# Kernel optimization log

Hardware: AMD Instinct MI355X
Metric: run time of the kernel (lower is better)

## Reference

```python
import jax, jax.numpy as jnp
import numpy as np

N_QUBITS = 12
DEPTH = 4
OUT_DIM = 2
HID = 64
BATCH = 4096


def _u3(a, b, c):
    """Combined RZ(c) @ RY(b) @ RX(a) single-qubit gate, batched. a,b,c: [B] -> [B,2,2] complex."""
    ca, sa = jnp.cos(a / 2), jnp.sin(a / 2)
    cb, sb = jnp.cos(b / 2), jnp.sin(b / 2)
    RX = jnp.stack([jnp.stack([ca + 0j, -1j * sa], -1),
                    jnp.stack([-1j * sa, ca + 0j], -1)], -2)
    RY = jnp.stack([jnp.stack([cb + 0j, -sb + 0j], -1),
                    jnp.stack([sb + 0j, cb + 0j], -1)], -2)
    ez = jnp.exp(-1j * c / 2)
    zeros = jnp.zeros_like(ez)
    RZ = jnp.stack([jnp.stack([ez, zeros], -1),
                    jnp.stack([zeros, jnp.conj(ez)], -1)], -2)
    return jnp.einsum('bij,bjk,bkl->bil', RZ, RY, RX)


def _apply_1q(psi, U, q):
    """psi: [B]+[2]*n (wire 0 = most significant), U: [B,2,2]."""
    psi = jnp.moveaxis(psi, q + 1, 1)
    shp = psi.shape
    psi = psi.reshape(shp[0], 2, -1)
    psi = jnp.einsum('bij,bjr->bir', U, psi)
    return jnp.moveaxis(psi.reshape(shp), 1, q + 1)


def _apply_cnot(psi, c, t):
    """CNOT with control c, target t on psi [B]+[2]*n."""
    s0 = jax.lax.index_in_dim(psi, 0, axis=c + 1, keepdims=True)
    s1 = jax.lax.index_in_dim(psi, 1, axis=c + 1, keepdims=True)
    s1 = jnp.flip(s1, axis=t + 1)
    return jnp.concatenate([s0, s1], axis=c + 1)


def _circuit_expvals(params):
    """Batched hardware-efficient ansatz state-vector sim.
    params: [B, DEPTH, N_QUBITS, 3] -> PauliZ expvals [B, N_QUBITS]."""
    B = params.shape[0]
    n = N_QUBITS
    psi = jnp.zeros((B, 2 ** n), jnp.complex64).at[:, 0].set(1.0)
    psi = psi.reshape((B,) + (2,) * n)
    for l in range(DEPTH):
        for q in range(n):  # RX, RY, RZ per qubit (fused to one 2x2)
            U = _u3(params[:, l, q, 0], params[:, l, q, 1], params[:, l, q, 2])
            psi = _apply_1q(psi, U, q)
        for q in range(n):   # ring of CNOTs
            psi = _apply_cnot(psi, q, (q + 1) % n)
    probs = (psi.real ** 2 + psi.imag ** 2).reshape(B, 2 ** n)
    idx = jnp.arange(2 ** n)
    bits = (idx[None, :] >> (n - 1 - jnp.arange(n))[:, None]) & 1  # [n, 2^n]
    signs = (1.0 - 2.0 * bits).astype(jnp.float32)
    return probs @ signs.T  # <Z_q> = p(bit=0) - p(bit=1)


def setup_inputs() -> dict:
    key = jax.random.key(0)
    ks = jax.random.split(key, 5)
    n = N_QUBITS
    n_params = DEPTH * n * 3
    def w(k, shape):
        return (jax.random.normal(k, shape, jnp.float32) / np.sqrt(shape[0])).astype(jnp.float32)
    return {
        'noise': jax.random.normal(ks[0], (BATCH, n), jnp.float32),
        'W1': w(ks[1], (n, HID)), 'b1': jnp.zeros((HID,), jnp.float32),
        'W2': w(ks[2], (HID, n_params)), 'b2': jnp.zeros((n_params,), jnp.float32),
        'W3': w(ks[3], (n, HID)), 'b3': jnp.zeros((HID,), jnp.float32),
        'W4': w(ks[4], (HID, OUT_DIM)), 'b4': jnp.zeros((OUT_DIM,), jnp.float32),
    }


def reference(noise, W1, b1, W2, b2, W3, b3, W4, b4):
    h = jnp.tanh(noise @ W1 + b1)
    circ_params = (h @ W2 + b2).reshape(noise.shape[0], DEPTH, N_QUBITS, 3)
    meas = _circuit_expvals(circ_params)          # [B, n_qubits]
    h2 = jnp.tanh(meas @ W3 + b3)
    return h2 @ W4 + b4                            # [B, output_dim]
```

## Files before the change

kernel.cpp:

```cpp
#include <hip/hip_runtime.h>
#include <math.h>

#define NQ  12
#define TPB 256

typedef __attribute__((ext_vector_type(2))) float f2;


struct GF12 { unsigned row[12]; };

constexpr GF12 gf_id(){ GF12 m{}; for(int i=0;i<12;i++) m.row[i]=1u<<i; return m; }
constexpr GF12 gf_mul(const GF12&A,const GF12&B){
  GF12 r{};
  for(int i=0;i<12;i++){ unsigned acc=0;
    for(int k=0;k<12;k++) if((A.row[i]>>k)&1u) acc ^= B.row[k];
    r.row[i]=acc; }
  return r;
}
constexpr unsigned gf_apply(const GF12&A, unsigned x){
  unsigned y=0;
  for(int i=0;i<12;i++) y |= (unsigned)(__builtin_popcount(A.row[i]&x)&1)<<i;
  return y;
}
constexpr GF12 gf_cnot(int q){ GF12 m=gf_id(); int c=11-q, t=11-((q+1)%12); m.row[t]^=(1u<<c); return m; }
constexpr GF12 gf_inv(const GF12&A){
  unsigned a[12], inv[12];
  for(int i=0;i<12;i++){ a[i]=A.row[i]; inv[i]=1u<<i; }
  for(int c=0;c<12;c++){
    int p=-1;
    for(int r2=c;r2<12;r2++) if((a[r2]>>c)&1u){p=r2;break;}
    if(p<0) continue;
    unsigned ta=a[c]; a[c]=a[p]; a[p]=ta;
    unsigned ti=inv[c]; inv[c]=inv[p]; inv[p]=ti;
    for(int r2=0;r2<12;r2++) if(r2!=c && ((a[r2]>>c)&1u)){ a[r2]^=a[c]; inv[r2]^=inv[c]; }
  }
  GF12 R{}; for(int i=0;i<12;i++) R.row[i]=inv[i];
  return R;
}

struct Red { unsigned arr[12]; int hb[12]; int n; };
constexpr unsigned red_reduce(const Red& R, unsigned y){
  for(int i=0;i<R.n;i++) if((y>>R.hb[i])&1u) y ^= R.arr[i];
  return y;
}
constexpr bool red_add(Red& R, unsigned cand){
  unsigned y = red_reduce(R, cand);
  if(!y) return false;
  int h=0;
  for(int b2=11;b2>=1;b2--) if((y>>b2)&1u){ h=b2; break; }
  R.arr[R.n]=y; R.hb[R.n]=h; R.n++;
  return true;
}

struct PairT {
  unsigned M0[4], M1[4];
  unsigned sz[16], gx[16];
  unsigned rB[8], roff[16];
};
struct AllT { PairT pr[6]; unsigned mq[12], uq[12]; bool ok; };

constexpr AllT makeAll(){
  AllT T{}; T.ok=true;
  GF12 D=gf_id(); for(int q=0;q<12;q++) D=gf_mul(gf_cnot(q),D);
  GF12 Cm=gf_id(); for(int q=11;q>=0;q--) Cm=gf_mul(gf_cnot(q),Cm);
  unsigned V[12][4]{},R[12][4]{},rfin[12]{};
  GF12 Mm=gf_id(), Mi=gf_id();
  for(int l=0;l<4;l++){
    for(int q=0;q<12;q++){
      int b=11-q; unsigned v=0;
      for(int j=0;j<12;j++) v|=((Mi.row[j]>>b)&1u)<<j;
      V[l*3+q/4][q&3]=v; R[l*3+q/4][q&3]=Mm.row[b];
    }
    Mm=gf_mul(D,Mm); Mi=gf_mul(Cm,Mi);
  }
  for(int q=0;q<12;q++) rfin[q]=Mm.row[11-q];

  GF12 Sg=gf_id(); Sg.row[1]|=1u<<4; Sg.row[2]|=1u<<5; Sg.row[3]|=1u<<6;

  GF12 Tprev{}, Tprev_inv{};
  for(int m=0;m<6;m++){
    const int p0=2*m, p1=p0+1;
    for(int pp=p0;pp<=p1;pp++) for(int j=0;j<4;j++) for(int i=0;i<4;i++){
      int par=__builtin_popcount(R[pp][j]&V[pp][i])&1;
      if(par!=((i==j)?1:0)) T.ok=false;
    }
    Red S{};
    for(int i=0;i<4;i++){ red_add(S,V[p0][i]); red_add(S,V[p1][i]); }
    for(unsigned x=1;x<4096 && S.n<10;x++) red_add(S,x);
    if(S.n!=10) T.ok=false;
    Red S12=S, RA{}, RB{};
    for(int i=0;i<4;i++){ red_add(RA,V[p0][i]); red_add(RB,V[p1][i]); }
    unsigned B[8]{};
    Red resR{};
    for(int k=0;k<6;k++){
      unsigned pick=0;
      if(m>0){
        unsigned res=(k<4)?(1u<<k):0u;
        for(unsigned hi=(k<4)?0u:1u; hi<256 && !pick; hi++){
          unsigned y=res|(hi<<4);
          unsigned x=gf_apply(Tprev_inv,y);
          if(red_reduce(S,x)) continue;
          if(!red_reduce(RA,x)) continue;
          if(!red_reduce(RB,x)) continue;
          pick=x;
        }
        for(unsigned y=1;y<4096 && !pick;y++){
          unsigned x=gf_apply(Tprev_inv,y);
          if(red_reduce(S,x)) continue;
          if(!red_reduce(RA,x)) continue;
          if(!red_reduce(RB,x)) continue;
          if(k<4){ unsigned rb=y&15u; if(!rb || !red_reduce(resR,rb)) continue; }
          pick=x;
        }
      }
      if(!pick){
        for(unsigned x=1;x<4096 && !pick;x++){
          if(red_reduce(S,x)) continue;
          if(!red_reduce(RA,x)) continue;
          if(!red_reduce(RB,x)) continue;
          pick=x;
        }
      }
      if(!pick){ T.ok=false; pick=1; }
      if(m>0 && k<4){ unsigned rb=gf_apply(Tprev,pick)&15u; if(rb) red_add(resR,rb); }
      red_add(RA,pick); red_add(RB,pick);
      B[k]=pick;
    }
    for(int k=6;k<8;k++){
      unsigned pick=0;
      for(unsigned x=1;x<4096 && !pick;x++) if(red_reduce(S12,x)) pick=x;
      if(!pick){ T.ok=false; pick=1; }
      red_add(S12,pick); B[k]=pick;
    }
    if(S12.n!=12) T.ok=false;
    GF12 Z{};
    for(int i=0;i<12;i++){
      unsigned rr=0;
      for(int k=0;k<4;k++) rr |= ((V[p1][k]>>i)&1u)<<k;
      for(int k=0;k<8;k++) rr |= ((B[k]>>i)&1u)<<(4+k);
      Z.row[i]=rr;
    }
    GF12 Tp=gf_inv(Z);
    { GF12 I2=gf_mul(Tp,Z); for(int i=0;i<12;i++) if(I2.row[i]!=(1u<<i)) T.ok=false; }
    for(int j=0;j<4;j++){
      unsigned m0=0,m1=0;
      for(int k=0;k<8;k++){
        m0 |= (unsigned)(__builtin_popcount(R[p0][j]&B[k])&1)<<k;
        m1 |= (unsigned)(__builtin_popcount(R[p1][j]&B[k])&1)<<k;
      }
      T.pr[m].M0[j]=m0; T.pr[m].M1[j]=m1;
    }
    unsigned zeta[4]{}, gam[4]{};
    for(int i=0;i<4;i++){
      unsigned d=gf_apply(Tp,V[p0][i]);
      if(d>>10) T.ok=false;
      zeta[i]=d&15u; gam[i]=(d>>4)&63u;
    }
    unsigned zmap[16]{}; bool seen[16]{};
    for(int z=0;z<16;z++){
      unsigned zz=0;
      for(int i=0;i<4;i++) if((z>>i)&1) zz^=zeta[i];
      zmap[z]=zz;
      if(seen[zz]) T.ok=false; seen[zz]=true;
    }
    for(int zp=0;zp<16;zp++){
      unsigned src=0;
      for(int z=0;z<16;z++) if(zmap[z]==(unsigned)zp) src=(unsigned)z;
      unsigned gg=0;
      for(int i=0;i<4;i++) if((src>>i)&1) gg^=gam[i];
      T.pr[m].sz[zp]=src; T.pr[m].gx[zp]=gg;
    }
    for(int z=0;z<16;z++){
      unsigned c0=0,c1=0,gg=0,bb=0;
      for(int i=0;i<4;i++){
        if((z>>i)&1){ c0^=V[p0][i]; gg^=gam[i]; }
        if((zmap[z]>>i)&1) c1^=V[p1][i];
      }
      for(int k=0;k<6;k++) if((gg>>k)&1) bb^=B[k];
      if((c0^c1^bb)!=0) T.ok=false;
    }
    if(m>0){
      for(int k=0;k<8;k++) T.pr[m].rB[k]=gf_apply(Tprev,B[k]);
      for(int z=0;z<16;z++){
        unsigned c=0;
        for(int i=0;i<4;i++) if((z>>i)&1) c^=V[p0][i];
        T.pr[m].roff[z]=gf_apply(Tprev,c);
      }
    }
    GF12 Tnew=gf_mul(Sg,Tp), Tnew_inv=gf_mul(Z,Sg);
    { GF12 I2=gf_mul(Tnew,Tnew_inv); for(int i=0;i<12;i++) if(I2.row[i]!=(1u<<i)) T.ok=false; }
    Tprev=Tnew; Tprev_inv=Tnew_inv;
    if(m==5){
      for(int q=0;q<12;q++){
        unsigned u=0,mm=0;
        for(int i=0;i<4;i++) u |= (unsigned)(__builtin_popcount(rfin[q]&V[11][i])&1)<<i;
        for(int k=0;k<8;k++) mm |= (unsigned)(__builtin_popcount(rfin[q]&B[k])&1)<<k;
        T.uq[q]=u; T.mq[q]=mm;
      }
    }
  }
  return T;
}

constexpr AllT hA = makeAll();
static_assert(hA.ok, "GF(2) paired-bpermute table self-check failed");

#define GATE_PK(SS,MM,JJ) do { \
    const int _lb = pl + 4*(JJ); \
    const unsigned _sg = ((unsigned)(__popc((MM) & (unsigned)t) & 1)) << 31; \
    const float _ar = __uint_as_float((unsigned)__builtin_amdgcn_readlane((int)cur, _lb+0)); \
    const float _ai = __uint_as_float(((unsigned)__builtin_amdgcn_readlane((int)cur, _lb+1)) ^ _sg); \
    const float _br = __uint_as_float(((unsigned)__builtin_amdgcn_readlane((int)cur, _lb+2)) ^ _sg); \
    const float _bi = __uint_as_float((unsigned)__builtin_amdgcn_readlane((int)cur, _lb+3)); \
    const f2 A0 = {_ar,_ar}, A1 = {-_ai,_ai}, B0 = {_br,_br}, B1 = {-_bi,_bi}; \
    _Pragma("unroll") \
    for (int s0=0; s0<16; ++s0){ \
      if ((s0 >> (JJ)) & 1) continue; \
      const int s1 = s0 | (1<<(JJ)); \
      const f2 X = SS[s0], Y = SS[s1]; \
      const f2 Xs = __builtin_shufflevector(X,X,1,0); \
      const f2 Ys = __builtin_shufflevector(Y,Y,1,0); \
      SS[s0] = __builtin_elementwise_fma(A0,X, \
               __builtin_elementwise_fma(A1,Xs, \
               __builtin_elementwise_fma(B0,Y, B1*Ys))); \
      SS[s1] = __builtin_elementwise_fma(A0,Y, \
               __builtin_elementwise_fma(-A1,Ys, \
               __builtin_elementwise_fma(-B0,X, B1*Xs))); \
    } \
  } while(0)

template<int M>
__device__ __forceinline__ void do_pair(f2 S[16], f2 Sn[16],
                                        unsigned c0, unsigned c1, unsigned c2,
                                        unsigned t, float2* s2, float4* s4)
{
  constexpr PairT P = hA.pr[M];
  if constexpr (M > 0){
    unsigned base=0;
    #pragma unroll
    for(int k=0;k<8;++k) base ^= ((t>>k)&1u) ? P.rB[k] : 0u;
    #pragma unroll
    for(int z=0;z<16;++z){ float2 v=s2[base ^ P.roff[z]]; S[z].x=v.x; S[z].y=v.y; }
  }
  { constexpr int ci=(2*M)>>2;
    const unsigned cur=(ci==0)?c0:((ci==1)?c1:c2);
    const int pl=((2*M)&3)<<4;
    GATE_PK(S,P.M0[0],0); GATE_PK(S,P.M0[1],1); GATE_PK(S,P.M0[2],2); GATE_PK(S,P.M0[3],3); }
  { const unsigned t4=t<<2;
    #pragma unroll
    for(int zp=0; zp<16; ++zp){
      const int idx=(int)(t4 ^ (P.gx[zp]<<2));
      Sn[zp].x=__uint_as_float((unsigned)__builtin_amdgcn_ds_bpermute(idx,(int)__float_as_uint(S[P.sz[zp]].x)));
      Sn[zp].y=__uint_as_float((unsigned)__builtin_amdgcn_ds_bpermute(idx,(int)__float_as_uint(S[P.sz[zp]].y)));
    } }
  { constexpr int ci=(2*M+1)>>2;
    const unsigned cur=(ci==0)?c0:((ci==1)?c1:c2);
    const int pl=((2*M+1)&3)<<4;
    GATE_PK(Sn,P.M1[0],0); GATE_PK(Sn,P.M1[1],1); GATE_PK(Sn,P.M1[2],2); GATE_PK(Sn,P.M1[3],3); }
  if constexpr (M < 5){
    __syncthreads();
    const unsigned wb=t<<3;
    #pragma unroll
    for(int k=0;k<8;++k)
      s4[wb | ((unsigned)k ^ (t&7u))] =
        make_float4(Sn[2*k].x, Sn[2*k].y, Sn[2*k+1].x, Sn[2*k+1].y);
    __syncthreads();
  }
}

__global__ void __launch_bounds__(TPB, 5)
qgen(const float* __restrict__ noise,
     const float* __restrict__ W1, const float* __restrict__ b1,
     const float* __restrict__ W2, const float* __restrict__ b2,
     const float* __restrict__ W3, const float* __restrict__ b3,
     const float* __restrict__ W4, const float* __restrict__ b4,
     float* __restrict__ out)
{
  __shared__ float2 s2[4096];
  float*  sf=(float*)s2;
  float4* s4=(float4*)s2;

  const unsigned t = threadIdx.x;
  const int b = blockIdx.x;
  const int lane = t & 63;

  if (t < 12) sf[400+t] = noise[b*12+t];
  __syncthreads();
  if (t < 64){
    float a = b1[t];
    #pragma unroll
    for (int k=0;k<12;++k) a = fmaf(sf[400+k], W1[k*64+t], a);
    sf[192+t] = tanhf(a);
  }
  __syncthreads();
  if (t < 144){
    float a = b2[t];
    #pragma unroll 16
    for (int j=0;j<64;++j) a = fmaf(sf[192+j], W2[j*144+t], a);
    sf[256+t] = a;
  }
  __syncthreads();
  if (t < 48){
    float aa = sf[256+3*t+0]*0.5f, bb = sf[256+3*t+1]*0.5f, c = sf[256+3*t+2]*0.5f;
    float sa,ca,sb,cb,sc2,cc;
    __sincosf(aa,&sa,&ca); __sincosf(bb,&sb,&cb); __sincosf(c,&sc2,&cc);
    float A=cb*ca, B=sb*sa, Cc=sb*ca, Dd=cb*sa;
    s4[t] = make_float4(fmaf(cc,A,  sc2*B),  fmaf(cc,B, -sc2*A),
                        fmaf(-cc,Cc,-sc2*Dd), fmaf(sc2,Cc,-cc*Dd));
  }
  __syncthreads();
  const unsigned* su=(const unsigned*)s2;
  const unsigned cu0=su[lane], cu1=su[64+lane], cu2=su[128+lane];
  __syncthreads();

  f2 S[16], Sn[16];
  #pragma unroll
  for(int k=0;k<16;++k){ S[k].x=0.f; S[k].y=0.f; }
  if(t==0) S[0].x=1.0f;

  do_pair<0>(S,Sn,cu0,cu1,cu2,t,s2,s4);
  do_pair<1>(S,Sn,cu0,cu1,cu2,t,s2,s4);
  do_pair<2>(S,Sn,cu0,cu1,cu2,t,s2,s4);
  do_pair<3>(S,Sn,cu0,cu1,cu2,t,s2,s4);
  do_pair<4>(S,Sn,cu0,cu1,cu2,t,s2,s4);
  do_pair<5>(S,Sn,cu0,cu1,cu2,t,s2,s4);

  float H[16];
  #pragma unroll
  for(int z=0;z<16;++z) H[z]=fmaf(Sn[z].x,Sn[z].x, Sn[z].y*Sn[z].y);
  #pragma unroll
  for(int st=1;st<16;st<<=1){
    #pragma unroll
    for(int z=0;z<16;++z){
      if(z & st) continue;
      float a0=H[z], a1=H[z|st];
      H[z]=a0+a1; H[z|st]=a0-a1;
    }
  }
  float acc[12];
  #pragma unroll
  for(int q=0;q<12;++q){
    const unsigned ls=((unsigned)(__popc(hA.mq[q]&t)&1))<<31;
    acc[q]=__uint_as_float(__float_as_uint(H[hA.uq[q]])^ls);
  }

  __syncthreads();
  const int wv=t>>6;
  #pragma unroll
  for(int q=0;q<12;++q){
    float v=acc[q];
    #pragma unroll
    for(int off=32;off>0;off>>=1) v += __shfl_down(v,off,64);
    if(lane==0) sf[wv*12+q]=v;
  }
  __syncthreads();
  if(t<12) sf[64+t]=sf[t]+sf[12+t]+sf[24+t]+sf[36+t];
  __syncthreads();

  if(t<64){
    float a=b3[t];
    #pragma unroll
    for(int k=0;k<12;++k) a=fmaf(sf[64+k],W3[k*64+t],a);
    float h2=tanhf(a);
    float p0=h2*W4[2*t+0], p1=h2*W4[2*t+1];
    #pragma unroll
    for(int off=32;off>0;off>>=1){ p0+=__shfl_down(p0,off,64); p1+=__shfl_down(p1,off,64); }
    if(t==0){ out[2*b+0]=p0+b4[0]; out[2*b+1]=p1+b4[1]; }
  }
}

extern "C" void kernel_launch(void* const* d_in, const int* in_sizes, int n_in,
                              void* d_out, int out_size, void* d_ws, size_t ws_size,
                              hipStream_t stream)
{
  const float* noise=(const float*)d_in[0];
  const float* W1=(const float*)d_in[1];
  const float* b1=(const float*)d_in[2];
  const float* W2=(const float*)d_in[3];
  const float* b2=(const float*)d_in[4];
  const float* W3=(const float*)d_in[5];
  const float* b3=(const float*)d_in[6];
  const float* W4=(const float*)d_in[7];
  const float* b4=(const float*)d_in[8];
  float* out=(float*)d_out;
  const int batch=in_sizes[0]/NQ;
  qgen<<<batch,TPB,0,stream>>>(noise,W1,b1,W2,b2,W3,b3,W4,b4,out);
}
```

Baseline: 200.4 us.

## Switch state-vector sim from radix-16 to radix-8 per thread with 512 threads

Each block now uses 512 threads holding 8 amplitudes each instead of 256 threads holding 16. Qubits are grouped in threes rather than fours, giving 8 paired stages instead of 6, and the GF(2) relabeling tables are regenerated for that grouping. The aim is to cut register pressure and raise per-block parallelism, hiding latency and allowing more waves per CU. The cost is more LDS exchange rounds and block-wide barriers, plus a wider final cross-wave reduction.

```diff
diff --git a/kernel.cpp b/kernel.cpp
--- a/kernel.cpp
+++ b/kernel.cpp
@@ -2,7 +2,7 @@
 #include <math.h>
 
 #define NQ  12
-#define TPB 256
+#define TPB 512
 
 typedef __attribute__((ext_vector_type(2))) float f2;
 
@@ -53,44 +53,55 @@
 }
 
 struct PairT {
-  unsigned M0[4], M1[4];
-  unsigned sz[16], gx[16];
-  unsigned rB[8], roff[16];
+  unsigned M0[3], M1[3];
+  unsigned sz[8], gx[8];
+  unsigned rB[9], roff[8];
 };
-struct AllT { PairT pr[6]; unsigned mq[12], uq[12]; bool ok; };
+struct AllT { PairT pr[8]; unsigned mq[12], uq[12]; bool ok; };
 
 constexpr AllT makeAll(){
   AllT T{}; T.ok=true;
   GF12 D=gf_id(); for(int q=0;q<12;q++) D=gf_mul(gf_cnot(q),D);
   GF12 Cm=gf_id(); for(int q=11;q>=0;q--) Cm=gf_mul(gf_cnot(q),Cm);
-  unsigned V[12][4]{},R[12][4]{},rfin[12]{};
+  unsigned V[16][3]{}, R[16][3]{}, rfin[12]{};
   GF12 Mm=gf_id(), Mi=gf_id();
   for(int l=0;l<4;l++){
     for(int q=0;q<12;q++){
       int b=11-q; unsigned v=0;
       for(int j=0;j<12;j++) v|=((Mi.row[j]>>b)&1u)<<j;
-      V[l*3+q/4][q&3]=v; R[l*3+q/4][q&3]=Mm.row[b];
+      V[4*l+q/3][q%3]=v; R[4*l+q/3][q%3]=Mm.row[b];
     }
     Mm=gf_mul(D,Mm); Mi=gf_mul(Cm,Mi);
   }
   for(int q=0;q<12;q++) rfin[q]=Mm.row[11-q];
 
-  GF12 Sg=gf_id(); Sg.row[1]|=1u<<4; Sg.row[2]|=1u<<5; Sg.row[3]|=1u<<6;
+  GF12 Sg=gf_id(); Sg.row[1]|=1u<<4; Sg.row[2]|=1u<<5;
 
   GF12 Tprev{}, Tprev_inv{};
-  for(int m=0;m<6;m++){
+  for(int m=0;m<8;m++){
     const int p0=2*m, p1=p0+1;
-    for(int pp=p0;pp<=p1;pp++) for(int j=0;j<4;j++) for(int i=0;i<4;i++){
+    for(int pp=p0;pp<=p1;pp++) for(int j=0;j<3;j++) for(int i=0;i<3;i++){
       int par=__builtin_popcount(R[pp][j]&V[pp][i])&1;
       if(par!=((i==j)?1:0)) T.ok=false;
     }
     Red S{};
-    for(int i=0;i<4;i++){ red_add(S,V[p0][i]); red_add(S,V[p1][i]); }
-    for(unsigned x=1;x<4096 && S.n<10;x++) red_add(S,x);
-    if(S.n!=10) T.ok=false;
-    Red S12=S, RA{}, RB{};
-    for(int i=0;i<4;i++){ red_add(RA,V[p0][i]); red_add(RB,V[p1][i]); }
-    unsigned B[8]{};
+    for(int i=0;i<3;i++){ red_add(S,V[p0][i]); red_add(S,V[p1][i]); }
+    if(S.n!=6) T.ok=false;
+    for(unsigned x=1;x<4096 && S.n<9;x++) red_add(S,x);
+    if(S.n!=9) T.ok=false;
+    unsigned W[3]{};
+    { Red SB=S;
+      for(int k=0;k<3;k++){
+        unsigned pick=0;
+        for(unsigned x=1;x<4096 && !pick;x++) if(red_reduce(SB,x)) pick=x;
+        if(!pick) T.ok=false; else red_add(SB,pick);
+        W[k]=pick;
+      }
+      if(SB.n!=12) T.ok=false;
+    }
+    Red RA{}, RB{};
+    for(int i=0;i<3;i++){ red_add(RA,V[p0][i]); red_add(RB,V[p1][i]); }
+    unsigned B[6]{};
     Red resR{};
     for(int k=0;k<6;k++){
       unsigned pick=0;
@@ -126,53 +137,52 @@
       red_add(RA,pick); red_add(RB,pick);
       B[k]=pick;
     }
-    for(int k=6;k<8;k++){
-      unsigned pick=0;
-      for(unsigned x=1;x<4096 && !pick;x++) if(red_reduce(S12,x)) pick=x;
-      if(!pick){ T.ok=false; pick=1; }
-      red_add(S12,pick); B[k]=pick;
-    }
-    if(S12.n!=12) T.ok=false;
+    if(RA.n!=9 || RB.n!=9) T.ok=false;
     GF12 Z{};
     for(int i=0;i<12;i++){
       unsigned rr=0;
-      for(int k=0;k<4;k++) rr |= ((V[p1][k]>>i)&1u)<<k;
-      for(int k=0;k<8;k++) rr |= ((B[k]>>i)&1u)<<(4+k);
+      for(int k=0;k<3;k++) rr |= ((V[p1][k]>>i)&1u)<<k;
+      for(int k=0;k<6;k++) rr |= ((B[k]>>i)&1u)<<(3+k);
+      for(int k=0;k<3;k++) rr |= ((W[k]>>i)&1u)<<(9+k);
       Z.row[i]=rr;
     }
     GF12 Tp=gf_inv(Z);
     { GF12 I2=gf_mul(Tp,Z); for(int i=0;i<12;i++) if(I2.row[i]!=(1u<<i)) T.ok=false; }
-    for(int j=0;j<4;j++){
+    for(int j=0;j<3;j++){
       unsigned m0=0,m1=0;
-      for(int k=0;k<8;k++){
+      for(int k=0;k<6;k++){
         m0 |= (unsigned)(__builtin_popcount(R[p0][j]&B[k])&1)<<k;
         m1 |= (unsigned)(__builtin_popcount(R[p1][j]&B[k])&1)<<k;
       }
+      for(int k=0;k<3;k++){
+        m0 |= (unsigned)(__builtin_popcount(R[p0][j]&W[k])&1)<<(6+k);
+        m1 |= (unsigned)(__builtin_popcount(R[p1][j]&W[k])&1)<<(6+k);
+      }
       T.pr[m].M0[j]=m0; T.pr[m].M1[j]=m1;
     }
-    unsigned zeta[4]{}, gam[4]{};
-    for(int i=0;i<4;i++){
+    unsigned zeta[3]{}, gam[3]{};
+    for(int i=0;i<3;i++){
       unsigned d=gf_apply(Tp,V[p0][i]);
-      if(d>>10) T.ok=false;
-      zeta[i]=d&15u; gam[i]=(d>>4)&63u;
-    }
-    unsigned zmap[16]{}; bool seen[16]{};
-    for(int z=0;z<16;z++){
+      if(d>>9) T.ok=false;
+      zeta[i]=d&7u; gam[i]=(d>>3)&63u;
+    }
+    unsigned zmap[8]{}; bool seen[8]{};
+    for(int z=0;z<8;z++){
       unsigned zz=0;
-      for(int i=0;i<4;i++) if((z>>i)&1) zz^=zeta[i];
+      for(int i=0;i<3;i++) if((z>>i)&1) zz^=zeta[i];
       zmap[z]=zz;
       if(seen[zz]) T.ok=false; seen[zz]=true;
     }
-    for(int zp=0;zp<16;zp++){
+    for(int zp=0;zp<8;zp++){
       unsigned src=0;
-      for(int z=0;z<16;z++) if(zmap[z]==(unsigned)zp) src=(unsigned)z;
+      for(int z=0;z<8;z++) if(zmap[z]==(unsigned)zp) src=(unsigned)z;
       unsigned gg=0;
-      for(int i=0;i<4;i++) if((src>>i)&1) gg^=gam[i];
+      for(int i=0;i<3;i++) if((src>>i)&1) gg^=gam[i];
       T.pr[m].sz[zp]=src; T.pr[m].gx[zp]=gg;
     }
-    for(int z=0;z<16;z++){
+    for(int z=0;z<8;z++){
       unsigned c0=0,c1=0,gg=0,bb=0;
-      for(int i=0;i<4;i++){
+      for(int i=0;i<3;i++){
         if((z>>i)&1){ c0^=V[p0][i]; gg^=gam[i]; }
         if((zmap[z]>>i)&1) c1^=V[p1][i];
       }
@@ -180,21 +190,23 @@
       if((c0^c1^bb)!=0) T.ok=false;
     }
     if(m>0){
-      for(int k=0;k<8;k++) T.pr[m].rB[k]=gf_apply(Tprev,B[k]);
-      for(int z=0;z<16;z++){
+      for(int k=0;k<6;k++) T.pr[m].rB[k]=gf_apply(Tprev,B[k]);
+      for(int k=0;k<3;k++) T.pr[m].rB[6+k]=gf_apply(Tprev,W[k]);
+      for(int z=0;z<8;z++){
         unsigned c=0;
-        for(int i=0;i<4;i++) if((z>>i)&1) c^=V[p0][i];
+        for(int i=0;i<3;i++) if((z>>i)&1) c^=V[p0][i];
         T.pr[m].roff[z]=gf_apply(Tprev,c);
       }
     }
     GF12 Tnew=gf_mul(Sg,Tp), Tnew_inv=gf_mul(Z,Sg);
     { GF12 I2=gf_mul(Tnew,Tnew_inv); for(int i=0;i<12;i++) if(I2.row[i]!=(1u<<i)) T.ok=false; }
     Tprev=Tnew; Tprev_inv=Tnew_inv;
-    if(m==5){
+    if(m==7){
       for(int q=0;q<12;q++){
         unsigned u=0,mm=0;
-        for(int i=0;i<4;i++) u |= (unsigned)(__builtin_popcount(rfin[q]&V[11][i])&1)<<i;
-        for(int k=0;k<8;k++) mm |= (unsigned)(__builtin_popcount(rfin[q]&B[k])&1)<<k;
+        for(int i=0;i<3;i++) u |= (unsigned)(__builtin_popcount(rfin[q]&V[15][i])&1)<<i;
+        for(int k=0;k<6;k++) mm |= (unsigned)(__builtin_popcount(rfin[q]&B[k])&1)<<k;
+        for(int k=0;k<3;k++) mm |= (unsigned)(__builtin_popcount(rfin[q]&W[k])&1)<<(6+k);
         T.uq[q]=u; T.mq[q]=mm;
       }
     }
@@ -203,18 +215,22 @@
 }
 
 constexpr AllT hA = makeAll();
-static_assert(hA.ok, "GF(2) paired-bpermute table self-check failed");
-
-#define GATE_PK(SS,MM,JJ) do { \
-    const int _lb = pl + 4*(JJ); \
-    const unsigned _sg = ((unsigned)(__popc((MM) & (unsigned)t) & 1)) << 31; \
-    const float _ar = __uint_as_float((unsigned)__builtin_amdgcn_readlane((int)cur, _lb+0)); \
-    const float _ai = __uint_as_float(((unsigned)__builtin_amdgcn_readlane((int)cur, _lb+1)) ^ _sg); \
-    const float _br = __uint_as_float(((unsigned)__builtin_amdgcn_readlane((int)cur, _lb+2)) ^ _sg); \
-    const float _bi = __uint_as_float((unsigned)__builtin_amdgcn_readlane((int)cur, _lb+3)); \
+static_assert(hA.ok, "GF(2) radix-8 paired table self-check failed");
+
+#define GATE_PK8(SS,PP,JJ,MM) do { \
+    constexpr int g_ = 12*((PP)/4) + 3*((PP)%4) + (JJ); \
+    constexpr int db_ = 4*g_; \
+    constexpr int rg_ = db_>>6; \
+    constexpr int di_ = db_&63; \
+    const unsigned cur = (rg_==0)?c0:((rg_==1)?c1:c2); \
+    const unsigned _sg = ((unsigned)(__popc((MM) & t) & 1)) << 31; \
+    const float _ar = __uint_as_float((unsigned)__builtin_amdgcn_readlane((int)cur, di_+0)); \
+    const float _ai = __uint_as_float(((unsigned)__builtin_amdgcn_readlane((int)cur, di_+1)) ^ _sg); \
+    const float _br = __uint_as_float(((unsigned)__builtin_amdgcn_readlane((int)cur, di_+2)) ^ _sg); \
+    const float _bi = __uint_as_float((unsigned)__builtin_amdgcn_readlane((int)cur, di_+3)); \
     const f2 A0 = {_ar,_ar}, A1 = {-_ai,_ai}, B0 = {_br,_br}, B1 = {-_bi,_bi}; \
     _Pragma("unroll") \
-    for (int s0=0; s0<16; ++s0){ \
+    for (int s0=0; s0<8; ++s0){ \
       if ((s0 >> (JJ)) & 1) continue; \
       const int s1 = s0 | (1<<(JJ)); \
       const f2 X = SS[s0], Y = SS[s1]; \
@@ -230,7 +246,7 @@
   } while(0)
 
 template<int M>
-__device__ __forceinline__ void do_pair(f2 S[16], f2 Sn[16],
+__device__ __forceinline__ void do_pair(f2 S[8], f2 Sn[8],
                                         unsigned c0, unsigned c1, unsigned c2,
                                         unsigned t, float2* s2, float4* s4)
 {
@@ -238,37 +254,32 @@
   if constexpr (M > 0){
     unsigned base=0;
     #pragma unroll
-    for(int k=0;k<8;++k) base ^= ((t>>k)&1u) ? P.rB[k] : 0u;
-    #pragma unroll
-    for(int z=0;z<16;++z){ float2 v=s2[base ^ P.roff[z]]; S[z].x=v.x; S[z].y=v.y; }
-  }
-  { constexpr int ci=(2*M)>>2;
-    const unsigned cur=(ci==0)?c0:((ci==1)?c1:c2);
-    const int pl=((2*M)&3)<<4;
-    GATE_PK(S,P.M0[0],0); GATE_PK(S,P.M0[1],1); GATE_PK(S,P.M0[2],2); GATE_PK(S,P.M0[3],3); }
-  { const unsigned t4=t<<2;
-    #pragma unroll
-    for(int zp=0; zp<16; ++zp){
-      const int idx=(int)(t4 ^ (P.gx[zp]<<2));
-      Sn[zp].x=__uint_as_float((unsigned)__builtin_amdgcn_ds_bpermute(idx,(int)__float_as_uint(S[P.sz[zp]].x)));
-      Sn[zp].y=__uint_as_float((unsigned)__builtin_amdgcn_ds_bpermute(idx,(int)__float_as_uint(S[P.sz[zp]].y)));
-    } }
-  { constexpr int ci=(2*M+1)>>2;
-    const unsigned cur=(ci==0)?c0:((ci==1)?c1:c2);
-    const int pl=((2*M+1)&3)<<4;
-    GATE_PK(Sn,P.M1[0],0); GATE_PK(Sn,P.M1[1],1); GATE_PK(Sn,P.M1[2],2); GATE_PK(Sn,P.M1[3],3); }
-  if constexpr (M < 5){
+    for(int k=0;k<9;++k) base ^= ((t>>k)&1u) ? P.rB[k] : 0u;
+    #pragma unroll
+    for(int z=0;z<8;++z){ float2 v=s2[base ^ P.roff[z]]; S[z].x=v.x; S[z].y=v.y; }
+  }
+  GATE_PK8(S,2*M,0,P.M0[0]); GATE_PK8(S,2*M,1,P.M0[1]); GATE_PK8(S,2*M,2,P.M0[2]);
+  #pragma unroll
+  for(int zp=0; zp<8; ++zp){
+    const int idx=(int)((((t)&63u) ^ P.gx[zp])<<2);
+    Sn[zp].x=__uint_as_float((unsigned)__builtin_amdgcn_ds_bpermute(idx,(int)__float_as_uint(S[P.sz[zp]].x)));
+    Sn[zp].y=__uint_as_float((unsigned)__builtin_amdgcn_ds_bpermute(idx,(int)__float_as_uint(S[P.sz[zp]].y)));
+  }
+  GATE_PK8(Sn,2*M+1,0,P.M1[0]); GATE_PK8(Sn,2*M+1,1,P.M1[1]); GATE_PK8(Sn,2*M+1,2,P.M1[2]);
+  if constexpr (M < 7){
     __syncthreads();
-    const unsigned wb=t<<3;
-    #pragma unroll
-    for(int k=0;k<8;++k)
-      s4[wb | ((unsigned)k ^ (t&7u))] =
-        make_float4(Sn[2*k].x, Sn[2*k].y, Sn[2*k+1].x, Sn[2*k+1].y);
+    const unsigned sw = ((t>>1)&3u)<<1;
+    #pragma unroll
+    for(int k=0;k<4;++k){
+      const unsigned z0 = 2u*(unsigned)k;
+      s4[(t<<2) | ((z0 ^ sw)>>1)] =
+        make_float4(Sn[z0].x, Sn[z0].y, Sn[z0|1u].x, Sn[z0|1u].y);
+    }
     __syncthreads();
   }
 }
 
-__global__ void __launch_bounds__(TPB, 5)
+__global__ void __launch_bounds__(TPB, 8)
 qgen(const float* __restrict__ noise,
      const float* __restrict__ W1, const float* __restrict__ b1,
      const float* __restrict__ W2, const float* __restrict__ b2,
@@ -310,28 +321,30 @@
   }
   __syncthreads();
   const unsigned* su=(const unsigned*)s2;
-  const unsigned cu0=su[lane], cu1=su[64+lane], cu2=su[128+lane];
-  __syncthreads();
-
-  f2 S[16], Sn[16];
-  #pragma unroll
-  for(int k=0;k<16;++k){ S[k].x=0.f; S[k].y=0.f; }
+  const unsigned c0=su[lane], c1=su[64+lane], c2=su[128+lane];
+  __syncthreads();
+
+  f2 S[8], Sn[8];
+  #pragma unroll
+  for(int k=0;k<8;++k){ S[k].x=0.f; S[k].y=0.f; }
   if(t==0) S[0].x=1.0f;
 
-  do_pair<0>(S,Sn,cu0,cu1,cu2,t,s2,s4);
-  do_pair<1>(S,Sn,cu0,cu1,cu2,t,s2,s4);
-  do_pair<2>(S,Sn,cu0,cu1,cu2,t,s2,s4);
-  do_pair<3>(S,Sn,cu0,cu1,cu2,t,s2,s4);
-  do_pair<4>(S,Sn,cu0,cu1,cu2,t,s2,s4);
-  do_pair<5>(S,Sn,cu0,cu1,cu2,t,s2,s4);
-
-  float H[16];
-  #pragma unroll
-  for(int z=0;z<16;++z) H[z]=fmaf(Sn[z].x,Sn[z].x, Sn[z].y*Sn[z].y);
-  #pragma unroll
-  for(int st=1;st<16;st<<=1){
-    #pragma unroll
-    for(int z=0;z<16;++z){
+  do_pair<0>(S,Sn,c0,c1,c2,t,s2,s4);
+  do_pair<1>(S,Sn,c0,c1,c2,t,s2,s4);
+  do_pair<2>(S,Sn,c0,c1,c2,t,s2,s4);
+  do_pair<3>(S,Sn,c0,c1,c2,t,s2,s4);
+  do_pair<4>(S,Sn,c0,c1,c2,t,s2,s4);
+  do_pair<5>(S,Sn,c0,c1,c2,t,s2,s4);
+  do_pair<6>(S,Sn,c0,c1,c2,t,s2,s4);
+  do_pair<7>(S,Sn,c0,c1,c2,t,s2,s4);
+
+  float H[8];
+  #pragma unroll
+  for(int z=0;z<8;++z) H[z]=fmaf(Sn[z].x,Sn[z].x, Sn[z].y*Sn[z].y);
+  #pragma unroll
+  for(int st=1;st<8;st<<=1){
+    #pragma unroll
+    for(int z=0;z<8;++z){
       if(z & st) continue;
       float a0=H[z], a1=H[z|st];
       H[z]=a0+a1; H[z|st]=a0-a1;
@@ -354,13 +367,18 @@
     if(lane==0) sf[wv*12+q]=v;
   }
   __syncthreads();
-  if(t<12) sf[64+t]=sf[t]+sf[12+t]+sf[24+t]+sf[36+t];
+  if(t<12){
+    float s=0.f;
+    #pragma unroll
+    for(int w2=0;w2<8;++w2) s += sf[w2*12+t];
+    sf[96+t]=s;
+  }
   __syncthreads();
 
   if(t<64){
     float a=b3[t];
     #pragma unroll
-    for(int k=0;k<12;++k) a=fmaf(sf[64+k],W3[k*64+t],a);
+    for(int k=0;k<12;++k) a=fmaf(sf[96+k],W3[k*64+t],a);
     float h2=tanhf(a);
     float p0=h2*W4[2*t+0], p1=h2*W4[2*t+1];
     #pragma unroll
```

Measured after the change: 218.0 us. 1.09x slower.
